# Kernel tuning notes

Hardware: AMD Instinct MI355X
Metric: run time of the kernel (lower is better)

The kernel has to match this reference:

```python
import jax, jax.numpy as jnp
import numpy as np
from jax import lax

B, Q, C, K = 256, 900, 91, 300  # batch, queries, classes, topk boxes for eval
SIGMA = 0.5                      # gaussian decay variance
SCORE_THR = 1e-3                 # hardcoded score_threshold in soft_nms


def setup_inputs() -> dict:
    key = jax.random.key(0)
    k1, k2, k3 = jax.random.split(key, 3)
    pred_logits = jax.random.normal(k1, (B, Q, C), dtype=jnp.float32)
    pred_boxes = jax.random.uniform(k2, (B, Q, 4), dtype=jnp.float32)  # cxcywh in [0,1]
    target_sizes = jax.random.randint(k3, (B, 2), 480, 1334).astype(jnp.float32)  # (h, w)
    return {"pred_logits": pred_logits, "pred_boxes": pred_boxes, "target_sizes": target_sizes}


def _iou_one(box, boxes):
    # box: [4] xyxy, boxes: [K,4] xyxy -> iou: [K]
    area1 = (box[2] - box[0]) * (box[3] - box[1])
    area2 = (boxes[:, 2] - boxes[:, 0]) * (boxes[:, 3] - boxes[:, 1])
    lt = jnp.maximum(box[:2], boxes[:, :2])
    rb = jnp.minimum(box[2:], boxes[:, 2:])
    wh = jnp.clip(rb - lt, 0.0)
    inter = wh[:, 0] * wh[:, 1]
    return inter / (area1 + area2 - inter)


def _soft_nms(boxes, scores):
    # boxes: [K,4], scores: [K]. Sequential gaussian soft-NMS, faithful to source
    # (source's iou_threshold arg is unused; decay applied to all trailing boxes).
    idxs = jnp.arange(K)

    def step(carry, i):
        bxs, scs, active = carry
        m = jnp.argmax(jnp.where(idxs >= i, scs, -jnp.inf))
        cond = active & (scs[m] >= SCORE_THR)  # break condition (sticky)
        # swap rows i <-> m
        bi, bm = bxs[i], bxs[m]
        si, sm = scs[i], scs[m]
        b2 = bxs.at[i].set(bm).at[m].set(bi)
        s2 = scs.at[i].set(sm).at[m].set(si)
        # gaussian decay on boxes after i
        decay = jnp.exp(-(_iou_one(b2[i], b2) ** 2) / SIGMA)
        s2 = s2 * jnp.where(idxs > i, decay, 1.0)
        return (jnp.where(cond, b2, bxs), jnp.where(cond, s2, scs), cond), None

    (boxes, scores, _), _ = lax.scan(step, (boxes, scores, jnp.array(True)), idxs)
    keep = scores > SCORE_THR
    return boxes, scores, keep


def _postprocess(pred_logits, pred_boxes, target_sizes):
    prob = jax.nn.sigmoid(pred_logits)                       # [B,Q,C]
    flat = prob.reshape(B, Q * C)
    topk_values, topk_indexes = lax.top_k(flat, K)           # [B,K]
    scores = topk_values
    topk_boxes = topk_indexes // C                           # query index
    labels = topk_indexes % C                                # class index
    # cxcywh -> xyxy
    cx, cy, w, h = jnp.split(pred_boxes, 4, axis=-1)
    xyxy = jnp.concatenate([cx - 0.5 * w, cy - 0.5 * h, cx + 0.5 * w, cy + 0.5 * h], axis=-1)
    gidx = jnp.broadcast_to(topk_boxes[..., None], (B, K, 4))
    boxes = jnp.take_along_axis(xyxy, gidx, axis=1)          # [B,K,4]
    img_h, img_w = target_sizes[:, 0], target_sizes[:, 1]
    scale = jnp.stack([img_w, img_h, img_w, img_h], axis=1)[:, None, :]
    boxes = boxes * scale
    boxes, scores, keep = jax.vmap(_soft_nms)(boxes, scores)
    return scores, labels, boxes, keep


def reference(pred_logits, pred_boxes, target_sizes):
    # Returns dense arrays + keep mask (ragged filtering expressed as a boolean mask
    # to stay jit-compatible). labels are intentionally NOT reordered by soft-NMS
    # swaps, matching the source's in-place mutation semantics.
    return _postprocess(pred_logits, pred_boxes, target_sizes)
```

## Files before the change

### kernel.cpp

```cpp
#include <hip/hip_runtime.h>
#include <cfloat>
#include <cmath>

#pragma clang fp contract(off)

#define BB 256
#define QQ 900
#define CC 91
#define KK 300
#define QC 81900
#define MAXIDX 81899
#define NF4 20475
#define STRIPC 30
#define SKCAP 512

#define OFF_SCORES 0
#define OFF_LABELS 76800
#define OFF_BOXES  153600
#define OFF_KEEP   460800

__device__ __forceinline__ unsigned int wave_max_u32(unsigned int x) {
#define DPP_MAX(ctrl, rmask)                                                   \
  { unsigned int tmp = (unsigned int)__builtin_amdgcn_update_dpp(              \
        (int)x, (int)x, ctrl, rmask, 0xF, false);                              \
    x = tmp > x ? tmp : x; }
  DPP_MAX(0x111, 0xF)
  DPP_MAX(0x112, 0xF)
  DPP_MAX(0x114, 0xF)
  DPP_MAX(0x118, 0xF)
  DPP_MAX(0x142, 0xA)
  DPP_MAX(0x143, 0xC)
#undef DPP_MAX
  return (unsigned int)__builtin_amdgcn_readlane((int)x, 63);
}

__device__ __forceinline__ float rdlane_f(float x, int l) {
  return __uint_as_float(
      (unsigned int)__builtin_amdgcn_readlane((int)__float_as_uint(x), l));
}

__global__ __launch_bounds__(256, 1) void fused_kernel(
    const float* __restrict__ logits,
    const float* __restrict__ boxes_in,
    const float* __restrict__ tsizes,
    float* __restrict__ out)
{
  const int b = blockIdx.x;
  const int t = threadIdx.x;
  const int lane = t & 63;
  const int w = t >> 6;

  __shared__ unsigned int strip[STRIPC + 1][256];
  __shared__ int hist[2048];
  __shared__ int suffix[256];
  __shared__ unsigned long long skey[SKCAP];
  __shared__ float  sc_lds[KK];
  __shared__ float4 bx_lds[KK];
  __shared__ int cnt2, cstar_s, cutbin;

  if (t == 0) { cnt2 = 0; cstar_s = 0; cutbin = 0; }
  for (int i = t; i < 2048; i += 256) hist[i] = 0;
  __syncthreads();

  const float4* row = (const float4*)(logits + (size_t)b * QC);
  unsigned int nh = 0;

  float4 f[8];
#define PROC_ELEM(xv, idxv)                                                    \
  {                                                                            \
    bool hit = (xv) > 2.0f;                                                    \
    unsigned int pos = hit ? nh : (unsigned int)STRIPC;                        \
    strip[pos][t] = (unsigned int)(idxv);                                      \
    nh = hit ? nh + 1u : nh;                                                   \
    nh = nh > (unsigned int)STRIPC ? (unsigned int)STRIPC : nh;                \
  }

  for (int k0 = 0; k0 + 8 <= 79; k0 += 8) {
#pragma unroll
    for (int u = 0; u < 8; ++u) f[u] = row[t + (k0 + u) * 256];
#pragma unroll
    for (int u = 0; u < 8; ++u) {
      const int i4 = (t + (k0 + u) * 256) * 4;
      PROC_ELEM(f[u].x, i4 + 0)
      PROC_ELEM(f[u].y, i4 + 1)
      PROC_ELEM(f[u].z, i4 + 2)
      PROC_ELEM(f[u].w, i4 + 3)
    }
  }
  for (int k = 72; k < 79; ++k) {
    float4 x4 = row[t + k * 256];
    const int i4 = (t + k * 256) * 4;
    PROC_ELEM(x4.x, i4 + 0)
    PROC_ELEM(x4.y, i4 + 1)
    PROC_ELEM(x4.z, i4 + 2)
    PROC_ELEM(x4.w, i4 + 3)
  }
  if (t < NF4 - 79 * 256) {
    float4 x4 = row[t + 79 * 256];
    const int i4 = (t + 79 * 256) * 4;
    PROC_ELEM(x4.x, i4 + 0)
    PROC_ELEM(x4.y, i4 + 1)
    PROC_ELEM(x4.z, i4 + 2)
    PROC_ELEM(x4.w, i4 + 3)
  }
#undef PROC_ELEM

  const float* lrow = logits + (size_t)b * QC;
  for (unsigned int j = 0; j < nh; ++j) {
    unsigned int idx = strip[j][t];
    float x = lrow[idx];
    unsigned int bin = (__float_as_uint(x) - 0x40000000u) >> 13;
    bin = bin > 2047u ? 2047u : bin;
    atomicAdd(&hist[bin], 1);
  }
  __syncthreads();

  {
    int cs = 0;
#pragma unroll
    for (int k = 0; k < 8; ++k) cs += hist[t * 8 + k];
    suffix[t] = cs;
  }
  __syncthreads();
  for (int off = 1; off < 256; off <<= 1) {
    int add = (t + off < 256) ? suffix[t + off] : 0;
    __syncthreads();
    suffix[t] += add;
    __syncthreads();
  }
  if (suffix[t] >= KK && (t == 255 || suffix[t + 1] < KK)) cstar_s = t;
  __syncthreads();
  if (t == 0) {
    int cs = cstar_s;
    int acc = (cs < 255) ? suffix[cs + 1] : 0;
    for (int k = 7; k >= 0; --k) {
      acc += hist[cs * 8 + k];
      if (acc >= KK) { cutbin = cs * 8 + k; break; }
    }
  }
  __syncthreads();
  const int cb = cutbin;

  for (unsigned int j = 0; j < nh; ++j) {
    unsigned int idx = strip[j][t];
    float x = lrow[idx];
    unsigned int bin = (__float_as_uint(x) - 0x40000000u) >> 13;
    bin = bin > 2047u ? 2047u : bin;
    if ((int)bin >= cb) {
      float sgm = 1.0f / (1.0f + expf(-x));
      int p = atomicAdd(&cnt2, 1);
      if (p < SKCAP)
        skey[p] = ((unsigned long long)__float_as_uint(sgm) << 17) |
                  (unsigned long long)(MAXIDX - idx);
    }
  }
  __syncthreads();
  const int M = min(cnt2, SKCAP);

  const float img_h = tsizes[b * 2 + 0];
  const float img_w = tsizes[b * 2 + 1];
  for (int o = t; o < M; o += 256) {
    unsigned long long ko = skey[o];
    int r = 0;
    for (int k = 0; k < M; ++k) r += (skey[k] > ko) ? 1 : 0;
    if (r < KK) {
      unsigned int bits = (unsigned int)(ko >> 17);
      int idx = MAXIDX - (int)(ko & 0x1FFFFull);
      int q   = idx / CC;
      int lab = idx - q * CC;

      out[OFF_LABELS + b * KK + r] = (float)lab;
      sc_lds[r] = __uint_as_float(bits);

      float4 bxv = ((const float4*)boxes_in)[(size_t)b * QQ + q];
      float cx = bxv.x, cy = bxv.y, ww = bxv.z, hh = bxv.w;
      float4 bo;
      bo.x = (cx - 0.5f * ww) * img_w;
      bo.y = (cy - 0.5f * hh) * img_h;
      bo.z = (cx + 0.5f * ww) * img_w;
      bo.w = (cy + 0.5f * hh) * img_h;
      bx_lds[r] = bo;
    }
  }
  __syncthreads();

  if (w == 0) {
    float  sc[5];
    float4 bxr[5];
    float  a2[5];
#pragma unroll
    for (int j = 0; j < 5; ++j) {
      int e = j * 64 + lane;
      if (e < KK) { sc[j] = sc_lds[e]; bxr[j] = bx_lds[e]; }
      else        { sc[j] = 0.0f; bxr[j] = make_float4(0.f, 0.f, 0.f, 0.f); }
      a2[j] = (bxr[j].z - bxr[j].x) * (bxr[j].w - bxr[j].y);
    }

#pragma unroll
    for (int ji = 0; ji < 5; ++ji) {
      const int iiend = (ji == 4) ? 44 : 64;
#pragma unroll 1
      for (int ii = 0; ii < iiend; ++ii) {
        const int i = ji * 64 + ii;

        unsigned int lm = (lane >= ii) ? __float_as_uint(sc[ji]) : 0u;
#pragma unroll
        for (int jj = ji + 1; jj < 5; ++jj) {
          unsigned int v = __float_as_uint(sc[jj]);
          lm = v > lm ? v : lm;
        }
        const unsigned int wm = wave_max_u32(lm);
        const float sm = __uint_as_float(wm);
        if (!(sm >= 0.001f)) goto nms_done;

        int jstar = ji, lstar = 0;
        float4 bm;
        {
          bool found = false;
#pragma unroll
          for (int jj = ji; jj < 5; ++jj) {
            if (!found) {
              bool cand = (__float_as_uint(sc[jj]) == wm);
              if (jj == ji) cand = cand && (lane >= ii);
              unsigned long long mm = __ballot(cand);
              if (mm) {
                jstar = jj;
                lstar = __ffsll((long long)mm) - 1;
                bm.x = rdlane_f(bxr[jj].x, lstar);
                bm.y = rdlane_f(bxr[jj].y, lstar);
                bm.z = rdlane_f(bxr[jj].z, lstar);
                bm.w = rdlane_f(bxr[jj].w, lstar);
                found = true;
              }
            }
          }
        }

        const float si = rdlane_f(sc[ji], ii);
        const float ai = rdlane_f(a2[ji], ii);
        float4 bi;
        bi.x = rdlane_f(bxr[ji].x, ii);
        bi.y = rdlane_f(bxr[ji].y, ii);
        bi.z = rdlane_f(bxr[ji].z, ii);
        bi.w = rdlane_f(bxr[ji].w, ii);
        const float area1 = (bm.z - bm.x) * (bm.w - bm.y);

        if (lane == ii) { sc[ji] = sm; bxr[ji] = bm; a2[ji] = area1; }
#pragma unroll
        for (int jj = ji; jj < 5; ++jj)
          if (jj == jstar && lane == lstar) { sc[jj] = si; bxr[jj] = bi; a2[jj] = ai; }

#pragma unroll
        for (int jj = ji; jj < 5; ++jj) {
          const bool act = (jj > ji) || (lane > ii);
          float4 bb = bxr[jj];
          float ltx = fmaxf(bm.x, bb.x);
          float lty = fmaxf(bm.y, bb.y);
          float rbx = fminf(bm.z, bb.z);
          float rby = fminf(bm.w, bb.w);
          float whx = fmaxf(rbx - ltx, 0.0f);
          float why = fmaxf(rby - lty, 0.0f);
          float inter = whx * why;
          float iou = inter / ((area1 + a2[jj]) - inter);
          float d = expf(-(iou * iou) * 2.0f);
          sc[jj] = act ? sc[jj] * d : sc[jj];
        }
      }
    }
nms_done:
#pragma unroll
    for (int j = 0; j < 5; ++j) {
      int e = j * 64 + lane;
      if (e < KK) {
        out[OFF_SCORES + b * KK + e] = sc[j];
        ((float4*)(out + OFF_BOXES))[b * KK + e] = bxr[j];
        out[OFF_KEEP + b * KK + e] = (sc[j] > 0.001f) ? 1.0f : 0.0f;
      }
    }
  }
}

extern "C" void kernel_launch(void* const* d_in, const int* in_sizes, int n_in,
                              void* d_out, int out_size, void* d_ws, size_t ws_size,
                              hipStream_t stream) {
  const float* pred_logits = (const float*)d_in[0];
  const float* pred_boxes  = (const float*)d_in[1];
  const float* tsizes      = (const float*)d_in[2];
  float* out = (float*)d_out;
  (void)d_ws; (void)ws_size;

  fused_kernel<<<BB, 256, 0, stream>>>(pred_logits, pred_boxes, tsizes, out);
}
```

Baseline: 298.6 us.

## Split top-k selection and soft-NMS into two kernels with packed argmax

The fused kernel is split into a selection kernel, which writes the top-k scores and scaled boxes to workspace, and a separate NMS kernel that packs 16 images' waves into one 1024-thread block across 16 blocks. In the old kernel only one wave per block ran the sequential NMS while the other three waves sat idle. The argmax now uses a 64-bit key (score bits plus inverted index) reduced with DPP, which returns the lowest winning index directly and removes the ballot search. The cost is an extra launch and a round trip through global memory. Only 16 CUs are busy during NMS, so each wave's serial latency on a shared CU may go up.

```diff
diff --git a/kernel.cpp b/kernel.cpp
--- a/kernel.cpp
+++ b/kernel.cpp
@@ -19,19 +19,33 @@
 #define OFF_BOXES  153600
 #define OFF_KEEP   460800
 
-__device__ __forceinline__ unsigned int wave_max_u32(unsigned int x) {
-#define DPP_MAX(ctrl, rmask)                                                   \
-  { unsigned int tmp = (unsigned int)__builtin_amdgcn_update_dpp(              \
-        (int)x, (int)x, ctrl, rmask, 0xF, false);                              \
-    x = tmp > x ? tmp : x; }
-  DPP_MAX(0x111, 0xF)
-  DPP_MAX(0x112, 0xF)
-  DPP_MAX(0x114, 0xF)
-  DPP_MAX(0x118, 0xF)
-  DPP_MAX(0x142, 0xA)
-  DPP_MAX(0x143, 0xC)
-#undef DPP_MAX
-  return (unsigned int)__builtin_amdgcn_readlane((int)x, 63);
+#define WS_OFF_BOXES 307200
+
+#define THR_BITS 0x3A83126Fu
+
+__device__ __forceinline__ unsigned long long wave_max_u64(unsigned long long x) {
+#define DPP_STEP(ctrl, rmask)                                                  \
+  {                                                                            \
+    unsigned int lo = (unsigned int)x, hi = (unsigned int)(x >> 32);           \
+    unsigned int nlo = (unsigned int)__builtin_amdgcn_update_dpp(              \
+        (int)lo, (int)lo, ctrl, rmask, 0xF, false);                            \
+    unsigned int nhi = (unsigned int)__builtin_amdgcn_update_dpp(              \
+        (int)hi, (int)hi, ctrl, rmask, 0xF, false);                            \
+    unsigned long long o = ((unsigned long long)nhi << 32) | nlo;              \
+    x = o > x ? o : x;                                                         \
+  }
+  DPP_STEP(0x111, 0xF)
+  DPP_STEP(0x112, 0xF)
+  DPP_STEP(0x114, 0xF)
+  DPP_STEP(0x118, 0xF)
+  DPP_STEP(0x142, 0xA)
+  DPP_STEP(0x143, 0xC)
+#undef DPP_STEP
+  unsigned int rlo =
+      (unsigned int)__builtin_amdgcn_readlane((int)(unsigned int)x, 63);
+  unsigned int rhi =
+      (unsigned int)__builtin_amdgcn_readlane((int)(unsigned int)(x >> 32), 63);
+  return ((unsigned long long)rhi << 32) | rlo;
 }
 
 __device__ __forceinline__ float rdlane_f(float x, int l) {
@@ -39,23 +53,21 @@
       (unsigned int)__builtin_amdgcn_readlane((int)__float_as_uint(x), l));
 }
 
-__global__ __launch_bounds__(256, 1) void fused_kernel(
+__global__ __launch_bounds__(256, 1) void select_kernel(
     const float* __restrict__ logits,
     const float* __restrict__ boxes_in,
     const float* __restrict__ tsizes,
-    float* __restrict__ out)
+    float* __restrict__ out,
+    float* __restrict__ ws_scores,
+    float4* __restrict__ ws_boxes)
 {
   const int b = blockIdx.x;
   const int t = threadIdx.x;
-  const int lane = t & 63;
-  const int w = t >> 6;
 
   __shared__ unsigned int strip[STRIPC + 1][256];
   __shared__ int hist[2048];
   __shared__ int suffix[256];
   __shared__ unsigned long long skey[SKCAP];
-  __shared__ float  sc_lds[KK];
-  __shared__ float4 bx_lds[KK];
   __shared__ int cnt2, cstar_s, cutbin;
 
   if (t == 0) { cnt2 = 0; cstar_s = 0; cutbin = 0; }
@@ -170,7 +182,7 @@
       int lab = idx - q * CC;
 
       out[OFF_LABELS + b * KK + r] = (float)lab;
-      sc_lds[r] = __uint_as_float(bits);
+      ws_scores[b * KK + r] = __uint_as_float(bits);
 
       float4 bxv = ((const float4*)boxes_in)[(size_t)b * QQ + q];
       float cx = bxv.x, cy = bxv.y, ww = bxv.z, hh = bxv.w;
@@ -179,103 +191,111 @@
       bo.y = (cy - 0.5f * hh) * img_h;
       bo.z = (cx + 0.5f * ww) * img_w;
       bo.w = (cy + 0.5f * hh) * img_h;
-      bx_lds[r] = bo;
-    }
-  }
-  __syncthreads();
-
-  if (w == 0) {
-    float  sc[5];
-    float4 bxr[5];
-    float  a2[5];
-#pragma unroll
-    for (int j = 0; j < 5; ++j) {
-      int e = j * 64 + lane;
-      if (e < KK) { sc[j] = sc_lds[e]; bxr[j] = bx_lds[e]; }
-      else        { sc[j] = 0.0f; bxr[j] = make_float4(0.f, 0.f, 0.f, 0.f); }
-      a2[j] = (bxr[j].z - bxr[j].x) * (bxr[j].w - bxr[j].y);
-    }
-
-#pragma unroll
-    for (int ji = 0; ji < 5; ++ji) {
-      const int iiend = (ji == 4) ? 44 : 64;
+      ws_boxes[b * KK + r] = bo;
+    }
+  }
+}
+
+__global__ __launch_bounds__(1024, 1) void nms_kernel(
+    const float*  __restrict__ ws_scores,
+    const float4* __restrict__ ws_boxes,
+    float* __restrict__ out)
+{
+  const int wv   = threadIdx.x >> 6;
+  const int lane = threadIdx.x & 63;
+  const int b    = blockIdx.x * 16 + wv;
+
+  float  sc[5];
+  float4 bxr[5];
+  float  a2[5];
+  int    elo[5];
+#pragma unroll
+  for (int j = 0; j < 5; ++j) {
+    int e = j * 64 + lane;
+    if (e < KK) { sc[j] = ws_scores[b * KK + e]; bxr[j] = ws_boxes[b * KK + e]; }
+    else        { sc[j] = 0.0f; bxr[j] = make_float4(0.f, 0.f, 0.f, 0.f); }
+    a2[j] = (bxr[j].z - bxr[j].x) * (bxr[j].w - bxr[j].y);
+    elo[j] = 1023 - e;
+  }
+
+#pragma unroll
+  for (int ji = 0; ji < 5; ++ji) {
+    const int iiend = (ji == 4) ? 44 : 64;
 #pragma unroll 1
-      for (int ii = 0; ii < iiend; ++ii) {
-        const int i = ji * 64 + ii;
-
-        unsigned int lm = (lane >= ii) ? __float_as_uint(sc[ji]) : 0u;
-#pragma unroll
-        for (int jj = ji + 1; jj < 5; ++jj) {
-          unsigned int v = __float_as_uint(sc[jj]);
-          lm = v > lm ? v : lm;
-        }
-        const unsigned int wm = wave_max_u32(lm);
-        const float sm = __uint_as_float(wm);
-        if (!(sm >= 0.001f)) goto nms_done;
-
-        int jstar = ji, lstar = 0;
-        float4 bm;
-        {
-          bool found = false;
-#pragma unroll
-          for (int jj = ji; jj < 5; ++jj) {
-            if (!found) {
-              bool cand = (__float_as_uint(sc[jj]) == wm);
-              if (jj == ji) cand = cand && (lane >= ii);
-              unsigned long long mm = __ballot(cand);
-              if (mm) {
-                jstar = jj;
-                lstar = __ffsll((long long)mm) - 1;
-                bm.x = rdlane_f(bxr[jj].x, lstar);
-                bm.y = rdlane_f(bxr[jj].y, lstar);
-                bm.z = rdlane_f(bxr[jj].z, lstar);
-                bm.w = rdlane_f(bxr[jj].w, lstar);
-                found = true;
-              }
-            }
-          }
-        }
-
-        const float si = rdlane_f(sc[ji], ii);
-        const float ai = rdlane_f(a2[ji], ii);
-        float4 bi;
-        bi.x = rdlane_f(bxr[ji].x, ii);
-        bi.y = rdlane_f(bxr[ji].y, ii);
-        bi.z = rdlane_f(bxr[ji].z, ii);
-        bi.w = rdlane_f(bxr[ji].w, ii);
-        const float area1 = (bm.z - bm.x) * (bm.w - bm.y);
-
-        if (lane == ii) { sc[ji] = sm; bxr[ji] = bm; a2[ji] = area1; }
-#pragma unroll
-        for (int jj = ji; jj < 5; ++jj)
-          if (jj == jstar && lane == lstar) { sc[jj] = si; bxr[jj] = bi; a2[jj] = ai; }
-
-#pragma unroll
-        for (int jj = ji; jj < 5; ++jj) {
-          const bool act = (jj > ji) || (lane > ii);
-          float4 bb = bxr[jj];
-          float ltx = fmaxf(bm.x, bb.x);
-          float lty = fmaxf(bm.y, bb.y);
-          float rbx = fminf(bm.z, bb.z);
-          float rby = fminf(bm.w, bb.w);
-          float whx = fmaxf(rbx - ltx, 0.0f);
-          float why = fmaxf(rby - lty, 0.0f);
-          float inter = whx * why;
-          float iou = inter / ((area1 + a2[jj]) - inter);
-          float d = expf(-(iou * iou) * 2.0f);
-          sc[jj] = act ? sc[jj] * d : sc[jj];
-        }
+    for (int ii = 0; ii < iiend; ++ii) {
+      unsigned long long k =
+          (lane >= ii)
+              ? ((((unsigned long long)__float_as_uint(sc[ji])) << 10) |
+                 (unsigned long long)elo[ji])
+              : 0ull;
+#pragma unroll
+      for (int jj = ji + 1; jj < 5; ++jj) {
+        unsigned long long kk =
+            (((unsigned long long)__float_as_uint(sc[jj])) << 10) |
+            (unsigned long long)elo[jj];
+        k = kk > k ? kk : k;
       }
-    }
+      const unsigned long long best = wave_max_u64(k);
+      const unsigned int wm = (unsigned int)(best >> 10);
+      if (wm < THR_BITS) goto nms_done;
+      const float sm = __uint_as_float(wm);
+      const int estar = 1023 - (int)(best & 1023ull);
+      const int jstar = estar >> 6;
+      const int lstar = estar & 63;
+
+      float4 bm;
+      switch (jstar) {
+        case 0: bm.x = rdlane_f(bxr[0].x, lstar); bm.y = rdlane_f(bxr[0].y, lstar);
+                bm.z = rdlane_f(bxr[0].z, lstar); bm.w = rdlane_f(bxr[0].w, lstar); break;
+        case 1: bm.x = rdlane_f(bxr[1].x, lstar); bm.y = rdlane_f(bxr[1].y, lstar);
+                bm.z = rdlane_f(bxr[1].z, lstar); bm.w = rdlane_f(bxr[1].w, lstar); break;
+        case 2: bm.x = rdlane_f(bxr[2].x, lstar); bm.y = rdlane_f(bxr[2].y, lstar);
+                bm.z = rdlane_f(bxr[2].z, lstar); bm.w = rdlane_f(bxr[2].w, lstar); break;
+        case 3: bm.x = rdlane_f(bxr[3].x, lstar); bm.y = rdlane_f(bxr[3].y, lstar);
+                bm.z = rdlane_f(bxr[3].z, lstar); bm.w = rdlane_f(bxr[3].w, lstar); break;
+        default: bm.x = rdlane_f(bxr[4].x, lstar); bm.y = rdlane_f(bxr[4].y, lstar);
+                 bm.z = rdlane_f(bxr[4].z, lstar); bm.w = rdlane_f(bxr[4].w, lstar); break;
+      }
+
+      const float si = rdlane_f(sc[ji], ii);
+      const float ai = rdlane_f(a2[ji], ii);
+      float4 bi;
+      bi.x = rdlane_f(bxr[ji].x, ii);
+      bi.y = rdlane_f(bxr[ji].y, ii);
+      bi.z = rdlane_f(bxr[ji].z, ii);
+      bi.w = rdlane_f(bxr[ji].w, ii);
+      const float area1 = (bm.z - bm.x) * (bm.w - bm.y);
+
+      if (lane == ii) { sc[ji] = sm; bxr[ji] = bm; a2[ji] = area1; }
+#pragma unroll
+      for (int jj = ji; jj < 5; ++jj)
+        if (jj == jstar && lane == lstar) { sc[jj] = si; bxr[jj] = bi; a2[jj] = ai; }
+
+#pragma unroll
+      for (int jj = ji; jj < 5; ++jj) {
+        const bool act = (jj > ji) || (lane > ii);
+        float4 bb = bxr[jj];
+        float ltx = fmaxf(bm.x, bb.x);
+        float lty = fmaxf(bm.y, bb.y);
+        float rbx = fminf(bm.z, bb.z);
+        float rby = fminf(bm.w, bb.w);
+        float whx = fmaxf(rbx - ltx, 0.0f);
+        float why = fmaxf(rby - lty, 0.0f);
+        float inter = whx * why;
+        float iou = inter / ((area1 + a2[jj]) - inter);
+        float d = expf(-(iou * iou) * 2.0f);
+        sc[jj] = act ? sc[jj] * d : sc[jj];
+      }
+    }
+  }
 nms_done:
 #pragma unroll
-    for (int j = 0; j < 5; ++j) {
-      int e = j * 64 + lane;
-      if (e < KK) {
-        out[OFF_SCORES + b * KK + e] = sc[j];
-        ((float4*)(out + OFF_BOXES))[b * KK + e] = bxr[j];
-        out[OFF_KEEP + b * KK + e] = (sc[j] > 0.001f) ? 1.0f : 0.0f;
-      }
+  for (int j = 0; j < 5; ++j) {
+    int e = j * 64 + lane;
+    if (e < KK) {
+      out[OFF_SCORES + b * KK + e] = sc[j];
+      ((float4*)(out + OFF_BOXES))[b * KK + e] = bxr[j];
+      out[OFF_KEEP + b * KK + e] = (sc[j] > 0.001f) ? 1.0f : 0.0f;
     }
   }
 }
@@ -287,7 +307,12 @@
   const float* pred_boxes  = (const float*)d_in[1];
   const float* tsizes      = (const float*)d_in[2];
   float* out = (float*)d_out;
-  (void)d_ws; (void)ws_size;
-
-  fused_kernel<<<BB, 256, 0, stream>>>(pred_logits, pred_boxes, tsizes, out);
-}
+
+  char* ws = (char*)d_ws;
+  float*  ws_scores = (float*)ws;
+  float4* ws_boxes  = (float4*)(ws + WS_OFF_BOXES);
+
+  select_kernel<<<BB, 256, 0, stream>>>(pred_logits, pred_boxes, tsizes,
+                                        out, ws_scores, ws_boxes);
+  nms_kernel<<<16, 1024, 0, stream>>>(ws_scores, ws_boxes, out);
+}
```

New measurement: 583.5 us. 1.95x slower.
